# Kernel tuning notes

Measured on AMD Instinct MI355X. Metric: run time of the kernel, lower is better.

## Reference

```python
import jax, jax.numpy as jnp
import numpy as np

VTH = 1.0          # firing threshold
SG_ALPHA = 4.0     # surrogate-gradient sharpness
TAU_MEM = 20.0

@jax.custom_vjp
def spike_fn(v):
    # Heaviside spike: 1 where membrane exceeds 0 (v is already v_mem - VTH)
    return (v > 0.0).astype(v.dtype)

def _spike_fwd(v):
    return spike_fn(v), v

def _spike_bwd(v, g):
    # sigmoid surrogate derivative: alpha * s * (1 - s)
    s = jax.nn.sigmoid(SG_ALPHA * v)
    return (g * SG_ALPHA * s * (1.0 - s),)

spike_fn.defvjp(_spike_fwd, _spike_bwd)

def lif_scan(h):
    # h: (batch, time, seq, hidden) -> spikes same shape, rate scalar
    beta = 1.0 - 1.0 / TAU_MEM  # membrane decay
    b, t, s, d = h.shape
    h_t = jnp.moveaxis(h, 1, 0)  # (time, batch, seq, hidden)

    def step(v, inp):
        v = beta * v + inp
        spk = spike_fn(v - VTH)
        v = v * (1.0 - spk)  # hard reset
        return v, spk

    v0 = jnp.zeros((b, s, d), dtype=h.dtype)
    _, spikes = jax.lax.scan(step, v0, h_t)
    spikes = jnp.moveaxis(spikes, 0, 1)  # (batch, time, seq, hidden)
    rate = spikes.mean()
    return spikes, rate

def setup_inputs() -> dict:
    key = jax.random.key(0)
    k1, k2, k3 = jax.random.split(key, 3)
    b, t, s, d = 16, 4, 256, 512
    hidden = 2048
    x = jax.random.normal(k1, (b, t, s, d), dtype=jnp.float32)
    # Kaiming-ish init so membrane inputs are O(1)
    w1 = jax.random.normal(k2, (hidden, d), dtype=jnp.float32) * (1.0 / np.sqrt(d))
    w2 = jax.random.normal(k3, (d, hidden), dtype=jnp.float32) * (1.0 / np.sqrt(hidden))
    return {"x": x, "w1": w1, "w2": w2}

def reference(x, w1, w2):
    # fc1: (b,t,s,d) @ (hidden,d)^T -> (b,t,s,hidden)
    h = jnp.einsum('btsd,hd->btsh', x, w1)
    spikes, rate = lif_scan(h)
    # fc2: (b,t,s,hidden) @ (d,hidden)^T -> (b,t,s,d)
    out = jnp.einsum('btsh,dh->btsd', spikes, w2)
    return out, rate
```

## Files before the change

kernel.cpp:

```cpp
#include <hip/hip_runtime.h>
#include <stdint.h>


typedef __attribute__((ext_vector_type(8))) short short8;
typedef __attribute__((ext_vector_type(4))) float f32x4;

#define AS1 __attribute__((address_space(1)))
#define AS3 __attribute__((address_space(3)))

__device__ __forceinline__ void load_lds16(const void* g, void* l) {
  __builtin_amdgcn_global_load_lds((const AS1 void*)g, (AS3 void*)l, 16, 0, 0);
}

__device__ __forceinline__ unsigned short f2bf(float f) {
  union { float f; unsigned u; } un; un.f = f;
  unsigned r = un.u + 0x7FFF + ((un.u >> 16) & 1);
  return (unsigned short)(r >> 16);
}
__device__ __forceinline__ float bf2f(unsigned short u) {
  union { unsigned u; float f; } un; un.u = ((unsigned)u) << 16; return un.f;
}

__global__ __launch_bounds__(256) void k0_split(
    const float* __restrict__ w2, unsigned short* __restrict__ hi,
    unsigned short* __restrict__ lo)
{
  int i = (blockIdx.x * 256 + threadIdx.x) * 4;
  float4 w = *(const float4*)&w2[i];
  unsigned short h4[4], l4[4];
  float ws[4] = {w.x, w.y, w.z, w.w};
#pragma unroll
  for (int c = 0; c < 4; ++c) {
    unsigned short h = f2bf(ws[c]);
    h4[c] = h;
    l4[c] = f2bf(ws[c] - bf2f(h));
  }
  *(ushort4*)&hi[i] = *(const ushort4*)h4;
  *(ushort4*)&lo[i] = *(const ushort4*)l4;
}

#define K1KT 32
#define PA 68
#define PB 132

__global__ __launch_bounds__(256) void k1_gemm_lif(
    const float* __restrict__ x,
    const float* __restrict__ w1,
    unsigned short* __restrict__ spikes,
    unsigned* __restrict__ cnt_out)
{
  __shared__ float sA[K1KT][PA];
  __shared__ float sB[K1KT][PB];

  const int tid = threadIdx.x;
  const int tx  = tid & 15;
  const int ty  = tid >> 4;

  const int bs0 = blockIdx.x * 64;
  const int h0  = blockIdx.y * 128;
  const int b   = bs0 >> 8;
  const int s0  = bs0 & 255;

  const int ar0 = tid >> 3;
  const int akc = (tid & 7) * 4;

  float v[4][8];
#pragma unroll
  for (int i = 0; i < 4; ++i)
#pragma unroll
    for (int j = 0; j < 8; ++j) v[i][j] = 0.0f;

  unsigned cnt = 0;

  for (int t = 0; t < 4; ++t) {
    const size_t arow0 = ((size_t)(b * 4 + t)) * 256 + s0;

    float acc[4][8];
#pragma unroll
    for (int i = 0; i < 4; ++i)
#pragma unroll
      for (int j = 0; j < 8; ++j) acc[i][j] = 0.0f;

    for (int k0 = 0; k0 < 512; k0 += K1KT) {
      __syncthreads();
#pragma unroll
      for (int j = 0; j < 2; ++j) {
        int r = ar0 + j * 32;
        float4 a = *(const float4*)&x[(arow0 + r) * 512 + k0 + akc];
        sA[akc + 0][r] = a.x; sA[akc + 1][r] = a.y;
        sA[akc + 2][r] = a.z; sA[akc + 3][r] = a.w;
      }
#pragma unroll
      for (int j = 0; j < 4; ++j) {
        int r = ar0 + j * 32;
        float4 wv = *(const float4*)&w1[(size_t)(h0 + r) * 512 + k0 + akc];
        sB[akc + 0][r] = wv.x; sB[akc + 1][r] = wv.y;
        sB[akc + 2][r] = wv.z; sB[akc + 3][r] = wv.w;
      }
      __syncthreads();

#pragma unroll
      for (int k = 0; k < K1KT; ++k) {
        float4 a4  = *(const float4*)&sA[k][ty * 4];
        float4 b4a = *(const float4*)&sB[k][tx * 4];
        float4 b4b = *(const float4*)&sB[k][64 + tx * 4];
        float aa[4] = {a4.x, a4.y, a4.z, a4.w};
        float ba[4] = {b4a.x, b4a.y, b4a.z, b4a.w};
        float bb[4] = {b4b.x, b4b.y, b4b.z, b4b.w};
#pragma unroll
        for (int i = 0; i < 4; ++i) {
#pragma unroll
          for (int j = 0; j < 4; ++j)
            acc[i][j] = __builtin_fmaf(aa[i], ba[j], acc[i][j]);
#pragma unroll
          for (int j = 0; j < 4; ++j)
            acc[i][4 + j] = __builtin_fmaf(aa[i], bb[j], acc[i][4 + j]);
        }
      }
    }

#pragma unroll
    for (int i = 0; i < 4; ++i) {
      unsigned short sp[8];
#pragma unroll
      for (int j = 0; j < 8; ++j) {
        float vv = __fmul_rn(0.95f, v[i][j]);
        vv = __fadd_rn(vv, acc[i][j]);
        bool s = vv > 1.0f;
        cnt += s ? 1u : 0u;
        v[i][j] = s ? 0.0f : vv;
        sp[j] = s ? (unsigned short)0x3F80 : (unsigned short)0;
      }
      unsigned short* row = spikes + (arow0 + ty * 4 + i) * 2048 + h0;
      *(ushort4*)&row[tx * 4]      = *(const ushort4*)&sp[0];
      *(ushort4*)&row[64 + tx * 4] = *(const ushort4*)&sp[4];
    }
  }

#pragma unroll
  for (int off = 32; off; off >>= 1) cnt += __shfl_down(cnt, off);
  if ((tid & 63) == 0) atomicAdd(cnt_out, cnt);
}

__global__ __launch_bounds__(256) void k2_gemm_mfma(
    const unsigned short* __restrict__ spikes,
    const unsigned short* __restrict__ w2h,
    const unsigned short* __restrict__ w2l,
    float* __restrict__ out)
{
  __shared__ alignas(16) short smA [128 * 64];
  __shared__ alignas(16) short smBh[128 * 64];
  __shared__ alignas(16) short smBl[128 * 64];

  const int tid  = threadIdx.x;
  const int lane = tid & 63;
  const int quad = lane >> 4;
  const int l15  = lane & 15;
  const int wv   = tid >> 6;
  const int wm   = wv & 1;
  const int wn   = wv >> 1;

  const size_t r0 = (size_t)blockIdx.x * 128;
  const int    d0 = blockIdx.y * 128;

  int srow[4], sg8[4];
#pragma unroll
  for (int j = 0; j < 4; ++j) {
    int gi  = j * 256 + tid;
    srow[j] = gi >> 3;
    sg8[j]  = ((gi & 7) ^ (srow[j] & 7)) * 8;
  }

  const unsigned short* ab  = spikes + r0 * 2048;
  const unsigned short* bhb = w2h + (size_t)d0 * 2048;
  const unsigned short* blb = w2l + (size_t)d0 * 2048;

  f32x4 acc[4][4] = {};

  for (int k0 = 0; k0 < 2048; k0 += 64) {
    __syncthreads();
#pragma unroll
    for (int j = 0; j < 4; ++j) {
      load_lds16(ab  + (size_t)srow[j] * 2048 + k0 + sg8[j],
                 &smA [(j * 256 + tid) * 8]);
      load_lds16(bhb + (size_t)srow[j] * 2048 + k0 + sg8[j],
                 &smBh[(j * 256 + tid) * 8]);
      load_lds16(blb + (size_t)srow[j] * 2048 + k0 + sg8[j],
                 &smBl[(j * 256 + tid) * 8]);
    }
    __syncthreads();

#pragma unroll
    for (int ks = 0; ks < 2; ++ks) {
      short8 af[4], bh[4], bl[4];
#pragma unroll
      for (int mi = 0; mi < 4; ++mi) {
        int m = wm * 64 + mi * 16 + l15;
        af[mi] = ((const short8*)smA)[m * 8 + ((ks * 4 + quad) ^ (m & 7))];
      }
#pragma unroll
      for (int ni = 0; ni < 4; ++ni) {
        int n = wn * 64 + ni * 16 + l15;
        int sl = n * 8 + ((ks * 4 + quad) ^ (n & 7));
        bh[ni] = ((const short8*)smBh)[sl];
        bl[ni] = ((const short8*)smBl)[sl];
      }
#pragma unroll
      for (int mi = 0; mi < 4; ++mi)
#pragma unroll
        for (int ni = 0; ni < 4; ++ni) {
          acc[mi][ni] = __builtin_amdgcn_mfma_f32_16x16x32_bf16(
              af[mi], bh[ni], acc[mi][ni], 0, 0, 0);
          acc[mi][ni] = __builtin_amdgcn_mfma_f32_16x16x32_bf16(
              af[mi], bl[ni], acc[mi][ni], 0, 0, 0);
        }
    }
  }

  float* ob = out + r0 * 512 + d0;
#pragma unroll
  for (int mi = 0; mi < 4; ++mi)
#pragma unroll
    for (int ni = 0; ni < 4; ++ni)
#pragma unroll
      for (int r = 0; r < 4; ++r) {
        int rr = wm * 64 + mi * 16 + quad * 4 + r;
        int cc = wn * 64 + ni * 16 + l15;
        ob[(size_t)rr * 512 + cc] = acc[mi][ni][r];
      }
}

#define KT 16
#define PADF 68

__global__ __launch_bounds__(256) void k2_gemm_valu(
    const unsigned short* __restrict__ spikes,
    const float* __restrict__ w2,
    float* __restrict__ out)
{
  __shared__ float sA[KT][PADF];
  __shared__ float sB[KT][PADF];

  const int tid = threadIdx.x;
  const int tx  = tid & 15;
  const int ty  = tid >> 4;
  const int lr  = tid >> 2;
  const int lg  = tid & 3;

  const size_t r0 = (size_t)blockIdx.x * 64;
  const int    d0 = blockIdx.y * 64;

  float acc[4][4];
#pragma unroll
  for (int i = 0; i < 4; ++i)
#pragma unroll
    for (int j = 0; j < 4; ++j) acc[i][j] = 0.0f;

  for (int k0 = 0; k0 < 2048; k0 += KT) {
    __syncthreads();
    ushort4 av = *(const ushort4*)&spikes[(r0 + lr) * 2048 + k0 + lg * 4];
    float4  bv = *(const float4*)&w2[(size_t)(d0 + lr) * 2048 + k0 + lg * 4];
    sA[lg * 4 + 0][lr] = bf2f(av.x); sA[lg * 4 + 1][lr] = bf2f(av.y);
    sA[lg * 4 + 2][lr] = bf2f(av.z); sA[lg * 4 + 3][lr] = bf2f(av.w);
    sB[lg * 4 + 0][lr] = bv.x; sB[lg * 4 + 1][lr] = bv.y;
    sB[lg * 4 + 2][lr] = bv.z; sB[lg * 4 + 3][lr] = bv.w;
    __syncthreads();

#pragma unroll
    for (int k = 0; k < KT; ++k) {
      float4 a4 = *(const float4*)&sA[k][ty * 4];
      float4 b4 = *(const float4*)&sB[k][tx * 4];
      float aa[4] = {a4.x, a4.y, a4.z, a4.w};
      float bb[4] = {b4.x, b4.y, b4.z, b4.w};
#pragma unroll
      for (int i = 0; i < 4; ++i)
#pragma unroll
        for (int j = 0; j < 4; ++j)
          acc[i][j] = __builtin_fmaf(aa[i], bb[j], acc[i][j]);
    }
  }

#pragma unroll
  for (int i = 0; i < 4; ++i) {
    float4 o = make_float4(acc[i][0], acc[i][1], acc[i][2], acc[i][3]);
    *(float4*)&out[(r0 + ty * 4 + i) * 512 + d0 + tx * 4] = o;
  }
}

__global__ void k3_rate(const unsigned* __restrict__ cnt, float* __restrict__ dst) {
  dst[0] = (float)((double)(*cnt) / 33554432.0);
}

extern "C" void kernel_launch(void* const* d_in, const int* in_sizes, int n_in,
                              void* d_out, int out_size, void* d_ws, size_t ws_size,
                              hipStream_t stream) {
  const float* x  = (const float*)d_in[0];
  const float* w1 = (const float*)d_in[1];
  const float* w2 = (const float*)d_in[2];
  float* out = (float*)d_out;

  unsigned* cnt = (unsigned*)d_ws;
  unsigned short* spikes = (unsigned short*)((char*)d_ws + 256);
  const size_t SPIKES_B = (size_t)16384 * 2048 * 2;
  unsigned short* w2h = (unsigned short*)((char*)d_ws + 256 + SPIKES_B);
  unsigned short* w2l = w2h + (size_t)512 * 2048;
  const size_t NEED_SPLIT = 256 + SPIKES_B + 2 * (size_t)512 * 2048 * 2;

  hipMemsetAsync(d_ws, 0, 256, stream);

  hipLaunchKernelGGL(k1_gemm_lif, dim3(64, 16), dim3(256), 0, stream,
                     x, w1, spikes, cnt);

  if (ws_size >= NEED_SPLIT) {
    hipLaunchKernelGGL(k0_split, dim3(1024), dim3(256), 0, stream, w2, w2h, w2l);
    hipLaunchKernelGGL(k2_gemm_mfma, dim3(128, 4), dim3(256), 0, stream,
                       spikes, w2h, w2l, out);
  } else {
    hipLaunchKernelGGL(k2_gemm_valu, dim3(256, 8), dim3(256), 0, stream,
                       spikes, w2, out);
  }

  hipLaunchKernelGGL(k3_rate, dim3(1), dim3(1), 0, stream, cnt, out + 8388608);
}
```

Measured before the change: 604.6 us.

## Compute all four timesteps in one fp32 GEMM tile with swizzled LDS

Restructures the fc1 GEMM so each block computes all four timesteps at once as a 256x128 tile, with each thread holding 16x8 accumulators. The LIF recurrence is then done across lanes with shuffles instead of looping over time. LDS is XOR-swizzled in place of padding to avoid bank conflicts, and both kernels gain a launch-bounds occupancy hint of 2. The aim is to raise the FMA-to-load ratio and load w1 once rather than four times. The risk is that 128 accumulators per thread cause register pressure or spills, and the hint of 2 may constrain register allocation.

```diff
diff --git a/kernel.cpp b/kernel.cpp
--- a/kernel.cpp
+++ b/kernel.cpp
@@ -40,101 +40,123 @@
 }
 
 #define K1KT 32
-#define PA 68
-#define PB 132
-
-__global__ __launch_bounds__(256) void k1_gemm_lif(
+#define SA_STR 256
+#define SB_STR 128
+
+__global__ __launch_bounds__(256, 2) void k1_gemm_lif(
     const float* __restrict__ x,
     const float* __restrict__ w1,
     unsigned short* __restrict__ spikes,
     unsigned* __restrict__ cnt_out)
 {
-  __shared__ float sA[K1KT][PA];
-  __shared__ float sB[K1KT][PB];
+  __shared__ float sA[K1KT * SA_STR];
+  __shared__ float sB[K1KT * SB_STR];
 
   const int tid = threadIdx.x;
   const int tx  = tid & 15;
   const int ty  = tid >> 4;
-
-  const int bs0 = blockIdx.x * 64;
-  const int h0  = blockIdx.y * 128;
-  const int b   = bs0 >> 8;
-  const int s0  = bs0 & 255;
-
-  const int ar0 = tid >> 3;
-  const int akc = (tid & 7) * 4;
-
-  float v[4][8];
-#pragma unroll
-  for (int i = 0; i < 4; ++i)
-#pragma unroll
-    for (int j = 0; j < 8; ++j) v[i][j] = 0.0f;
+  const int t   = ty & 3;
+  const int ssg = ty >> 2;
+
+  const int bx = blockIdx.x;
+  const int b  = bx >> 2;
+  const int s0 = (bx & 3) * 64;
+  const int h0 = blockIdx.y * 128;
+
+  const int u  = tid >> 3;
+  const int kg = tid & 7;
+
+  float acc[16][8];
+#pragma unroll
+  for (int i = 0; i < 16; ++i)
+#pragma unroll
+    for (int j = 0; j < 8; ++j) acc[i][j] = 0.0f;
+
+  const int aBase  = t * 64 + ssg * 16;
+  const int tXor   = 4 * t;
+  const int bBase0 = tx * 4;
+  const int bBase1 = 64 + tx * 4;
+
+  for (int k0 = 0; k0 < 512; k0 += K1KT) {
+    __syncthreads();
+
+#pragma unroll
+    for (int j = 0; j < 8; ++j) {
+      int r  = u + 32 * j;
+      int tr = r >> 6, ss = r & 63;
+      size_t grow = ((size_t)(b * 4 + tr) << 8) + s0 + ss;
+      float4 a = *(const float4*)&x[grow * 512 + k0 + kg * 4];
+      int sl = r ^ (4 * (kg ^ tr));
+      sA[(4 * kg + 0) * SA_STR + sl] = a.x;
+      sA[(4 * kg + 1) * SA_STR + sl] = a.y;
+      sA[(4 * kg + 2) * SA_STR + sl] = a.z;
+      sA[(4 * kg + 3) * SA_STR + sl] = a.w;
+    }
+#pragma unroll
+    for (int j = 0; j < 4; ++j) {
+      int c = u + 32 * j;
+      float4 wv = *(const float4*)&w1[(size_t)(h0 + c) * 512 + k0 + kg * 4];
+      int sl = c ^ (4 * kg);
+      sB[(4 * kg + 0) * SB_STR + sl] = wv.x;
+      sB[(4 * kg + 1) * SB_STR + sl] = wv.y;
+      sB[(4 * kg + 2) * SB_STR + sl] = wv.z;
+      sB[(4 * kg + 3) * SB_STR + sl] = wv.w;
+    }
+    __syncthreads();
+
+    for (int kk = 0; kk < K1KT; kk += 4) {
+      const int aXor = kk ^ tXor;
+      const int bXor = kk;
+#pragma unroll
+      for (int k2i = 0; k2i < 4; ++k2i) {
+        const int k = kk + k2i;
+        const float* aRow = &sA[k * SA_STR];
+        const float* bRow = &sB[k * SB_STR];
+        float4 a0 = *(const float4*)&aRow[(aBase + 0)  ^ aXor];
+        float4 a1 = *(const float4*)&aRow[(aBase + 4)  ^ aXor];
+        float4 a2 = *(const float4*)&aRow[(aBase + 8)  ^ aXor];
+        float4 a3 = *(const float4*)&aRow[(aBase + 12) ^ aXor];
+        float4 b0 = *(const float4*)&bRow[bBase0 ^ bXor];
+        float4 b1 = *(const float4*)&bRow[bBase1 ^ bXor];
+        float av[16] = {a0.x, a0.y, a0.z, a0.w, a1.x, a1.y, a1.z, a1.w,
+                        a2.x, a2.y, a2.z, a2.w, a3.x, a3.y, a3.z, a3.w};
+        float bv[8]  = {b0.x, b0.y, b0.z, b0.w, b1.x, b1.y, b1.z, b1.w};
+#pragma unroll
+        for (int i = 0; i < 16; ++i)
+#pragma unroll
+          for (int j = 0; j < 8; ++j)
+            acc[i][j] = __builtin_fmaf(av[i], bv[j], acc[i][j]);
+      }
+    }
+  }
 
   unsigned cnt = 0;
-
-  for (int t = 0; t < 4; ++t) {
-    const size_t arow0 = ((size_t)(b * 4 + t)) * 256 + s0;
-
-    float acc[4][8];
-#pragma unroll
-    for (int i = 0; i < 4; ++i)
-#pragma unroll
-      for (int j = 0; j < 8; ++j) acc[i][j] = 0.0f;
-
-    for (int k0 = 0; k0 < 512; k0 += K1KT) {
-      __syncthreads();
-#pragma unroll
-      for (int j = 0; j < 2; ++j) {
-        int r = ar0 + j * 32;
-        float4 a = *(const float4*)&x[(arow0 + r) * 512 + k0 + akc];
-        sA[akc + 0][r] = a.x; sA[akc + 1][r] = a.y;
-        sA[akc + 2][r] = a.z; sA[akc + 3][r] = a.w;
-      }
-#pragma unroll
-      for (int j = 0; j < 4; ++j) {
-        int r = ar0 + j * 32;
-        float4 wv = *(const float4*)&w1[(size_t)(h0 + r) * 512 + k0 + akc];
-        sB[akc + 0][r] = wv.x; sB[akc + 1][r] = wv.y;
-        sB[akc + 2][r] = wv.z; sB[akc + 3][r] = wv.w;
-      }
-      __syncthreads();
-
-#pragma unroll
-      for (int k = 0; k < K1KT; ++k) {
-        float4 a4  = *(const float4*)&sA[k][ty * 4];
-        float4 b4a = *(const float4*)&sB[k][tx * 4];
-        float4 b4b = *(const float4*)&sB[k][64 + tx * 4];
-        float aa[4] = {a4.x, a4.y, a4.z, a4.w};
-        float ba[4] = {b4a.x, b4a.y, b4a.z, b4a.w};
-        float bb[4] = {b4b.x, b4b.y, b4b.z, b4b.w};
-#pragma unroll
-        for (int i = 0; i < 4; ++i) {
-#pragma unroll
-          for (int j = 0; j < 4; ++j)
-            acc[i][j] = __builtin_fmaf(aa[i], ba[j], acc[i][j]);
-#pragma unroll
-          for (int j = 0; j < 4; ++j)
-            acc[i][4 + j] = __builtin_fmaf(aa[i], bb[j], acc[i][4 + j]);
-        }
-      }
-    }
-
-#pragma unroll
-    for (int i = 0; i < 4; ++i) {
-      unsigned short sp[8];
-#pragma unroll
-      for (int j = 0; j < 8; ++j) {
-        float vv = __fmul_rn(0.95f, v[i][j]);
-        vv = __fadd_rn(vv, acc[i][j]);
+#pragma unroll
+  for (int i = 0; i < 16; ++i) {
+    unsigned short sp[8];
+#pragma unroll
+    for (int j = 0; j < 8; ++j) {
+      float a = acc[i][j];
+      float h[4];
+#pragma unroll
+      for (int tt = 0; tt < 4; ++tt)
+        h[tt] = __shfl(a, tt * 16 + tx, 64);
+      float vv = 0.0f;
+      bool smine = false;
+#pragma unroll
+      for (int tt = 0; tt < 4; ++tt) {
+        vv = __fadd_rn(__fmul_rn(0.95f, vv), h[tt]);
         bool s = vv > 1.0f;
-        cnt += s ? 1u : 0u;
-        v[i][j] = s ? 0.0f : vv;
-        sp[j] = s ? (unsigned short)0x3F80 : (unsigned short)0;
-      }
-      unsigned short* row = spikes + (arow0 + ty * 4 + i) * 2048 + h0;
-      *(ushort4*)&row[tx * 4]      = *(const ushort4*)&sp[0];
-      *(ushort4*)&row[64 + tx * 4] = *(const ushort4*)&sp[4];
-    }
+        smine = (tt == t) ? s : smine;
+        vv = s ? 0.0f : vv;
+      }
+      cnt += smine ? 1u : 0u;
+      sp[j] = smine ? (unsigned short)0x3F80 : (unsigned short)0;
+    }
+    size_t grow = ((size_t)(b * 4 + t) << 8) + s0 + ssg * 16 + i;
+    unsigned short* rowp = spikes + grow * 2048 + h0;
+    *(ushort4*)&rowp[tx * 4]      = *(const ushort4*)&sp[0];
+    *(ushort4*)&rowp[64 + tx * 4] = *(const ushort4*)&sp[4];
   }
 
 #pragma unroll
@@ -142,7 +164,7 @@
   if ((tid & 63) == 0) atomicAdd(cnt_out, cnt);
 }
 
-__global__ __launch_bounds__(256) void k2_gemm_mfma(
+__global__ __launch_bounds__(256, 2) void k2_gemm_mfma(
     const unsigned short* __restrict__ spikes,
     const unsigned short* __restrict__ w2h,
     const unsigned short* __restrict__ w2l,
```

New measurement: 562.6 us. 1.07x faster.
